# Performance work log

Measured on AMD Instinct MI355X. Metric: run time of the kernel, lower is better.

The kernel has to match this reference:

```python
import jax, jax.numpy as jnp
import numpy as np

B, S, D, H = 4, 2048, 1024, 16
DK = D // H

def setup_inputs() -> dict:
    key = jax.random.key(0)
    ks = jax.random.split(key, 5)
    std = np.sqrt(2.0 / (D + D)).astype(np.float32)
    return {
        "x": jax.random.normal(ks[0], (B, S, D), dtype=jnp.float32),
        "W_q": jax.random.normal(ks[1], (D, D), dtype=jnp.float32) * std,
        "W_k": jax.random.normal(ks[2], (D, D), dtype=jnp.float32) * std,
        "W_v": jax.random.normal(ks[3], (D, D), dtype=jnp.float32) * std,
        "W_o": jax.random.normal(ks[4], (D, D), dtype=jnp.float32) * std,
    }

def reference(x, W_q, W_k, W_v, W_o):
    b, s, d = x.shape
    # Linear layers: y = x @ W.T  (W stored as [out, in])
    q = (x @ W_q.T).reshape(b, s, H, DK).transpose(0, 2, 1, 3)  # [b,h,s,dk]
    k = (x @ W_k.T).reshape(b, s, H, DK).transpose(0, 2, 1, 3)
    v = (x @ W_v.T).reshape(b, s, H, DK).transpose(0, 2, 1, 3)
    scale = 1.0 / jnp.sqrt(jnp.asarray(DK, dtype=x.dtype))
    scores = jnp.einsum("bhqd,bhkd->bhqk", q, k) * scale  # [b,h,s,s]
    causal = jnp.tril(jnp.ones((s, s), dtype=bool))
    scores = jnp.where(causal, scores, jnp.asarray(-jnp.inf, dtype=scores.dtype))
    attn = jax.nn.softmax(scores, axis=-1)
    out = jnp.einsum("bhqk,bhkd->bhqd", attn, v)  # [b,h,s,dk]
    out = out.transpose(0, 2, 1, 3).reshape(b, s, d)
    return out @ W_o.T
```

## Files before the change

kernel.cpp:

```cpp
#include <hip/hip_runtime.h>
#include <stdint.h>

#define B_  4
#define S_  2048
#define D_  1024
#define H_  16
#define DK_ 64
#define M_  (B_ * S_)

typedef __attribute__((ext_vector_type(4))) float  f32x4;
typedef __attribute__((ext_vector_type(8))) __bf16 bf16x8;
typedef __attribute__((ext_vector_type(4))) unsigned short us4;

__device__ __forceinline__ unsigned short cvt_bf16(float f) {
  unsigned u = __float_as_uint(f);
  return (unsigned short)((u + 0x7fffu + ((u >> 16) & 1u)) >> 16);
}

__device__ __forceinline__ f32x4 mfma16(bf16x8 a, bf16x8 b, f32x4 c) {
  return __builtin_amdgcn_mfma_f32_16x16x32_bf16(a, b, c, 0, 0, 0);
}

__device__ __forceinline__ void async16(const void* g, void* l) {
  __builtin_amdgcn_global_load_lds(
      (const __attribute__((address_space(1))) void*)g,
      (__attribute__((address_space(3))) void*)l, 16, 0, 0);
}

#define XN4_ 2097152
#define WN4_ 262144
__global__ void cast_all(const float* __restrict__ x,
                         const float* __restrict__ wq,
                         const float* __restrict__ wk,
                         const float* __restrict__ wv,
                         const float* __restrict__ wo,
                         unsigned short* __restrict__ dst) {
  const int i = blockIdx.x * blockDim.x + threadIdx.x;
  const float* src;
  int k;
  if (i < XN4_) {
    src = x; k = i;
  } else {
    const int j = i - XN4_;
    const int wsel = j >> 18;
    k = j & (WN4_ - 1);
    src = (wsel == 0) ? wq : (wsel == 1) ? wk : (wsel == 2) ? wv : wo;
  }
  f32x4 v = ((const f32x4*)src)[k];
  us4 o;
  o[0] = cvt_bf16(v[0]); o[1] = cvt_bf16(v[1]);
  o[2] = cvt_bf16(v[2]); o[3] = cvt_bf16(v[3]);
  ((us4*)dst)[i] = o;
}

template <int OUTMODE>
__global__ __launch_bounds__(256) void gemm_bt(
    const unsigned short* __restrict__ A,
    const unsigned short* __restrict__ Bm,
    void* __restrict__ Cp,
    unsigned short* __restrict__ Qo, unsigned short* __restrict__ Ko,
    unsigned short* __restrict__ Vto,
    int Ndim, int Kdim) {
  constexpr int BM = 128, BN = 128, BK = 32;
  __shared__ __align__(16) unsigned short As[BM * BK];
  __shared__ __align__(16) unsigned short Bs[BN * BK];

  const int tid = threadIdx.x;
  const int w = tid >> 6, l = tid & 63;
  const int l16 = l & 15, lg = l >> 4;
  const int wr = w >> 1, wc = w & 1;
  const int rowA0 = blockIdx.y * BM;
  const int rowB0 = blockIdx.x * BN;
  const int l4 = l >> 2;
  const int lk = (l & 3) * 8;

  f32x4 acc[4][4] = {};

  for (int kt = 0; kt < Kdim; kt += BK) {
#pragma unroll
    for (int j = 0; j < 2; ++j) {
      const int chunk = j * 4 + w;
      const int r = chunk * 16 + l4;
      async16(A  + (size_t)(rowA0 + r) * Kdim + kt + lk, &As[chunk * 512]);
      async16(Bm + (size_t)(rowB0 + r) * Kdim + kt + lk, &Bs[chunk * 512]);
    }
    __syncthreads();
    bf16x8 af[4], bfr[4];
#pragma unroll
    for (int m = 0; m < 4; ++m)
      af[m] = *(const bf16x8*)&As[(wr * 64 + m * 16 + l16) * BK + lg * 8];
#pragma unroll
    for (int n = 0; n < 4; ++n)
      bfr[n] = *(const bf16x8*)&Bs[(wc * 64 + n * 16 + l16) * BK + lg * 8];
#pragma unroll
    for (int m = 0; m < 4; ++m)
#pragma unroll
      for (int n = 0; n < 4; ++n)
        acc[m][n] = mfma16(af[m], bfr[n], acc[m][n]);
    __syncthreads();
  }

  const int rb = rowA0 + wr * 64;
  const int cb = rowB0 + wc * 64;
  if constexpr (OUTMODE == 2) {
    float* C = (float*)Cp;
#pragma unroll
    for (int m = 0; m < 4; ++m)
#pragma unroll
      for (int n = 0; n < 4; ++n) {
        const int r0 = rb + m * 16 + lg * 4;
        const int c0 = cb + n * 16 + l16;
#pragma unroll
        for (int j = 0; j < 4; ++j)
          C[(size_t)(r0 + j) * Ndim + c0] = acc[m][n][j];
      }
  } else {
    const int region = cb >> 10;
    const int cbl = cb & 1023;
    if (region < 2) {
      unsigned short* C = region ? Ko : Qo;
#pragma unroll
      for (int m = 0; m < 4; ++m)
#pragma unroll
        for (int n = 0; n < 4; ++n) {
          const int r0 = rb + m * 16 + lg * 4;
          const int c0 = cbl + n * 16 + l16;
#pragma unroll
          for (int j = 0; j < 4; ++j)
            C[(size_t)(r0 + j) * 1024 + c0] = cvt_bf16(acc[m][n][j]);
        }
    } else {
#pragma unroll
      for (int m = 0; m < 4; ++m)
#pragma unroll
        for (int n = 0; n < 4; ++n) {
          const int r0 = rb + m * 16 + lg * 4;
          const int c0 = cbl + n * 16 + l16;
          us4 v;
#pragma unroll
          for (int j = 0; j < 4; ++j) v[j] = cvt_bf16(acc[m][n][j]);
          *(us4*)&Vto[((size_t)(r0 >> 11) * 1024 + c0) * 2048 + (r0 & 2047)] = v;
        }
    }
  }
}


#define KS_ 0.1803368801f

#define SMX(sc, mr, sr, oa, P, diag, rb, kv0)                                \
  do {                                                                       \
    if (diag) {                                                              \
      _Pragma("unroll") for (int nc_ = 0; nc_ < 4; ++nc_) {                  \
        const int col_ = (kv0) + nc_ * 16 + l16;                             \
        _Pragma("unroll") for (int j_ = 0; j_ < 4; ++j_)                     \
            if (col_ > (rb) + j_) sc[nc_][j_] = -INFINITY;                   \
      }                                                                      \
    }                                                                        \
    _Pragma("unroll") for (int j_ = 0; j_ < 4; ++j_) {                       \
      float t_ = fmaxf(fmaxf(sc[0][j_], sc[1][j_]),                          \
                       fmaxf(sc[2][j_], sc[3][j_]));                         \
      t_ = fmaxf(t_, __shfl_xor(t_, 1));                                     \
      t_ = fmaxf(t_, __shfl_xor(t_, 2));                                     \
      t_ = fmaxf(t_, __shfl_xor(t_, 4));                                     \
      t_ = fmaxf(t_, __shfl_xor(t_, 8));                                     \
      const bool st_ = __all(t_ <= mr[j_]);     \
      const float mnew_ = st_ ? mr[j_] : fmaxf(mr[j_], t_);                  \
      float rs_ = 0.f;                                                       \
      _Pragma("unroll") for (int nc_ = 0; nc_ < 4; ++nc_) {                  \
        const float p_ = exp2f((sc[nc_][j_] - mnew_) * KS_);                 \
        rs_ += p_;                                                           \
        P[lg * 4 + j_][nc_ * 16 + l16] = cvt_bf16(p_);                       \
      }                                                                      \
      rs_ += __shfl_xor(rs_, 1);                                             \
      rs_ += __shfl_xor(rs_, 2);                                             \
      rs_ += __shfl_xor(rs_, 4);                                             \
      rs_ += __shfl_xor(rs_, 8);                                             \
      if (st_) {                                                             \
        sr[j_] += rs_;                                                       \
      } else {                                                               \
        const float al_ = exp2f((mr[j_] - mnew_) * KS_);                     \
        sr[j_] = sr[j_] * al_ + rs_;                                         \
        mr[j_] = mnew_;                                                      \
        _Pragma("unroll") for (int d_ = 0; d_ < 4; ++d_) oa[d_][j_] *= al_;  \
      }                                                                      \
    }                                                                        \
  } while (0)

__global__ __launch_bounds__(256, 4) void flash_attn(
    const unsigned short* __restrict__ Q,
    const unsigned short* __restrict__ K,
    const unsigned short* __restrict__ Vt,
    unsigned short* __restrict__ O) {
  const int bid  = blockIdx.x;
  const int virt = (bid & 7) * 128 + (bid >> 3);
  const int bh   = virt >> 4;
  const int x    = virt & 15;
  const int b = bh >> 4, h = bh & 15;
  const int tid = threadIdx.x;
  const int w = tid >> 6, l = tid & 63;
  const int l16 = l & 15, lg = l >> 4;

  __shared__ __align__(16) unsigned short Ks[64 * 64];
  __shared__ __align__(16) unsigned short Vs[64 * 64];
  __shared__ __align__(16) unsigned short PA[4][16][72];
  __shared__ __align__(16) unsigned short PB[4][16][72];

  const int tA = x, tB = 31 - x;

  const size_t qkbase = (size_t)(b * S_) * D_ + h * DK_;
  const size_t vbase  = ((size_t)(b * D_) + h * DK_) * S_;

  const int rA = tA * 64 + w * 16 + l16;
  const int rB = tB * 64 + w * 16 + l16;
  bf16x8 qfA[2], qfB[2];
  qfA[0] = *(const bf16x8*)&Q[qkbase + (size_t)rA * D_ + lg * 8];
  qfA[1] = *(const bf16x8*)&Q[qkbase + (size_t)rA * D_ + 32 + lg * 8];
  qfB[0] = *(const bf16x8*)&Q[qkbase + (size_t)rB * D_ + lg * 8];
  qfB[1] = *(const bf16x8*)&Q[qkbase + (size_t)rB * D_ + 32 + lg * 8];

  float mA[4], sA[4], mB[4], sB[4];
  f32x4 oA[4] = {}, oB[4] = {};
#pragma unroll
  for (int j = 0; j < 4; ++j) {
    mA[j] = mB[j] = -INFINITY;
    sA[j] = sB[j] = 0.f;
  }

  const int rbA = tA * 64 + w * 16 + lg * 4;
  const int rbB = tB * 64 + w * 16 + lg * 4;

  for (int kv = 0; kv <= tB; ++kv) {
    const int kv0 = kv * 64;
    if (kv) __syncthreads();
#pragma unroll
    for (int c = 0; c < 2; ++c) {
      const int ci = c * 256 + w * 64;
      const int i  = ci + l;
      const int r  = i >> 3;
      const int cc = (i & 7) ^ (r & 7);
      async16(K  + qkbase + (size_t)(kv0 + r) * D_ + cc * 8, &Ks[ci * 8]);
      async16(Vt + vbase  + (size_t)r * S_ + kv0 + cc * 8,   &Vs[ci * 8]);
    }
    __syncthreads();

    if (kv <= tA) {
      f32x4 sc[4] = {};
      __builtin_amdgcn_s_setprio(1);
#pragma unroll
      for (int nc = 0; nc < 4; ++nc) {
        const int r = nc * 16 + l16;
#pragma unroll
        for (int ks = 0; ks < 2; ++ks) {
          const int byte = (r * 128 + ks * 64 + lg * 16) ^ ((r & 7) << 4);
          bf16x8 kf = *(const bf16x8*)((const char*)Ks + byte);
          sc[nc] = mfma16(qfA[ks], kf, sc[nc]);
        }
      }
      __builtin_amdgcn_s_setprio(0);
      SMX(sc, mA, sA, oA, PA[w], kv == tA, rbA, kv0);
      __asm__ volatile("s_waitcnt lgkmcnt(0)" ::: "memory");
      bf16x8 pa0 = *(const bf16x8*)&PA[w][l16][lg * 8];
      bf16x8 pa1 = *(const bf16x8*)&PA[w][l16][32 + lg * 8];
      __builtin_amdgcn_s_setprio(1);
#pragma unroll
      for (int d = 0; d < 4; ++d) {
        const int r = d * 16 + l16;
#pragma unroll
        for (int ks = 0; ks < 2; ++ks) {
          const int byte = (r * 128 + ks * 64 + lg * 16) ^ ((r & 7) << 4);
          bf16x8 vf = *(const bf16x8*)((const char*)Vs + byte);
          oA[d] = mfma16(ks ? pa1 : pa0, vf, oA[d]);
        }
      }
      __builtin_amdgcn_s_setprio(0);
    }

    {
      f32x4 sc[4] = {};
      __builtin_amdgcn_s_setprio(1);
#pragma unroll
      for (int nc = 0; nc < 4; ++nc) {
        const int r = nc * 16 + l16;
#pragma unroll
        for (int ks = 0; ks < 2; ++ks) {
          const int byte = (r * 128 + ks * 64 + lg * 16) ^ ((r & 7) << 4);
          bf16x8 kf = *(const bf16x8*)((const char*)Ks + byte);
          sc[nc] = mfma16(qfB[ks], kf, sc[nc]);
        }
      }
      __builtin_amdgcn_s_setprio(0);
      SMX(sc, mB, sB, oB, PB[w], kv == tB, rbB, kv0);
      __asm__ volatile("s_waitcnt lgkmcnt(0)" ::: "memory");
      bf16x8 pb0 = *(const bf16x8*)&PB[w][l16][lg * 8];
      bf16x8 pb1 = *(const bf16x8*)&PB[w][l16][32 + lg * 8];
      __builtin_amdgcn_s_setprio(1);
#pragma unroll
      for (int d = 0; d < 4; ++d) {
        const int r = d * 16 + l16;
#pragma unroll
        for (int ks = 0; ks < 2; ++ks) {
          const int byte = (r * 128 + ks * 64 + lg * 16) ^ ((r & 7) << 4);
          bf16x8 vf = *(const bf16x8*)((const char*)Vs + byte);
          oB[d] = mfma16(ks ? pb1 : pb0, vf, oB[d]);
        }
      }
      __builtin_amdgcn_s_setprio(0);
    }
  }

#pragma unroll
  for (int j = 0; j < 4; ++j) {
    const float iA = __builtin_amdgcn_rcpf(sA[j]);
    const float iB = __builtin_amdgcn_rcpf(sB[j]);
#pragma unroll
    for (int d = 0; d < 4; ++d) {
      O[((size_t)(b * S_) + rbA + j) * D_ + h * DK_ + d * 16 + l16] =
          cvt_bf16(oA[d][j] * iA);
      O[((size_t)(b * S_) + rbB + j) * D_ + h * DK_ + d * 16 + l16] =
          cvt_bf16(oB[d][j] * iB);
    }
  }
}

extern "C" void kernel_launch(void* const* d_in, const int* in_sizes, int n_in,
                              void* d_out, int out_size, void* d_ws,
                              size_t ws_size, hipStream_t stream) {
  const float* x  = (const float*)d_in[0];
  const float* Wq = (const float*)d_in[1];
  const float* Wk = (const float*)d_in[2];
  const float* Wv = (const float*)d_in[3];
  const float* Wo = (const float*)d_in[4];

  const size_t XN = (size_t)M_ * D_;
  const size_t WN = (size_t)D_ * D_;
  unsigned short* xb  = (unsigned short*)d_ws;
  unsigned short* Wqb = xb + XN;
  unsigned short* Wob = Wqb + 3 * WN;
  unsigned short* Qb  = Wob + WN;
  unsigned short* Kb  = Qb + XN;
  unsigned short* Vtb = Kb + XN;
  unsigned short* Ob  = Vtb + XN;

  cast_all<<<(XN4_ + 4 * WN4_) / 256, 256, 0, stream>>>(x, Wq, Wk, Wv, Wo, xb);

  gemm_bt<3><<<dim3(24, 64), 256, 0, stream>>>(xb, Wqb, nullptr, Qb, Kb, Vtb,
                                               3072, D_);

  flash_attn<<<dim3(1024), 256, 0, stream>>>(Qb, Kb, Vtb, Ob);

  gemm_bt<2><<<dim3(8, 64), 256, 0, stream>>>(Ob, Wob, d_out, nullptr, nullptr,
                                              nullptr, D_, D_);
}
```

Before: 318.2 us.

## Double-buffer K/V tiles and interleave both query tiles per KV step

After: 410.1 us. +28.9%, slower.

```diff
diff --git a/kernel.cpp b/kernel.cpp
--- a/kernel.cpp
+++ b/kernel.cpp
@@ -187,7 +187,22 @@
     }                                                                        \
   } while (0)
 
-__global__ __launch_bounds__(256, 4) void flash_attn(
+#define STAGE(kvt, pb)                                                       \
+  do {                                                                       \
+    const int kv0_ = (kvt) * 64;                                             \
+    _Pragma("unroll") for (int c_ = 0; c_ < 2; ++c_) {                       \
+      const int ci_ = c_ * 256 + w * 64;                                     \
+      const int i_  = ci_ + l;                                               \
+      const int r_  = i_ >> 3;                                               \
+      const int cc_ = (i_ & 7) ^ (r_ & 7);                                   \
+      async16(K  + qkbase + (size_t)(kv0_ + r_) * D_ + cc_ * 8,              \
+              &Ks[pb][ci_ * 8]);                                             \
+      async16(Vt + vbase  + (size_t)r_ * S_ + kv0_ + cc_ * 8,                \
+              &Vs[pb][ci_ * 8]);                                             \
+    }                                                                        \
+  } while (0)
+
+__global__ __launch_bounds__(256, 3) void flash_attn(
     const unsigned short* __restrict__ Q,
     const unsigned short* __restrict__ K,
     const unsigned short* __restrict__ Vt,
@@ -201,8 +216,8 @@
   const int w = tid >> 6, l = tid & 63;
   const int l16 = l & 15, lg = l >> 4;
 
-  __shared__ __align__(16) unsigned short Ks[64 * 64];
-  __shared__ __align__(16) unsigned short Vs[64 * 64];
+  __shared__ __align__(16) unsigned short Ks[2][64 * 64];
+  __shared__ __align__(16) unsigned short Vs[2][64 * 64];
   __shared__ __align__(16) unsigned short PA[4][16][72];
   __shared__ __align__(16) unsigned short PB[4][16][72];
 
@@ -230,83 +245,55 @@
   const int rbA = tA * 64 + w * 16 + lg * 4;
   const int rbB = tB * 64 + w * 16 + lg * 4;
 
+  STAGE(0, 0);
+  __syncthreads();
+
   for (int kv = 0; kv <= tB; ++kv) {
+    const int p = kv & 1;
     const int kv0 = kv * 64;
-    if (kv) __syncthreads();
-#pragma unroll
-    for (int c = 0; c < 2; ++c) {
-      const int ci = c * 256 + w * 64;
-      const int i  = ci + l;
-      const int r  = i >> 3;
-      const int cc = (i & 7) ^ (r & 7);
-      async16(K  + qkbase + (size_t)(kv0 + r) * D_ + cc * 8, &Ks[ci * 8]);
-      async16(Vt + vbase  + (size_t)r * S_ + kv0 + cc * 8,   &Vs[ci * 8]);
+    if (kv < tB) STAGE(kv + 1, p ^ 1);
+
+    const bool doA = (kv <= tA);
+    const char* Kp = (const char*)&Ks[p][0];
+    const char* Vp = (const char*)&Vs[p][0];
+
+    f32x4 scA[4] = {}, scB[4] = {};
+#pragma unroll
+    for (int nc = 0; nc < 4; ++nc) {
+      const int r = nc * 16 + l16;
+#pragma unroll
+      for (int ks = 0; ks < 2; ++ks) {
+        const int byte = (r * 128 + ks * 64 + lg * 16) ^ ((r & 7) << 4);
+        bf16x8 kf = *(const bf16x8*)(Kp + byte);
+        if (doA) scA[nc] = mfma16(qfA[ks], kf, scA[nc]);
+        scB[nc] = mfma16(qfB[ks], kf, scB[nc]);
+      }
+    }
+
+    if (doA) SMX(scA, mA, sA, oA, PA[w], kv == tA, rbA, kv0);
+    SMX(scB, mB, sB, oB, PB[w], kv == tB, rbB, kv0);
+
+    __asm__ volatile("s_waitcnt lgkmcnt(0)" ::: "memory");
+    bf16x8 paA0, paA1, paB0, paB1;
+    if (doA) {
+      paA0 = *(const bf16x8*)&PA[w][l16][lg * 8];
+      paA1 = *(const bf16x8*)&PA[w][l16][32 + lg * 8];
+    }
+    paB0 = *(const bf16x8*)&PB[w][l16][lg * 8];
+    paB1 = *(const bf16x8*)&PB[w][l16][32 + lg * 8];
+
+#pragma unroll
+    for (int d = 0; d < 4; ++d) {
+      const int r = d * 16 + l16;
+#pragma unroll
+      for (int ks = 0; ks < 2; ++ks) {
+        const int byte = (r * 128 + ks * 64 + lg * 16) ^ ((r & 7) << 4);
+        bf16x8 vf = *(const bf16x8*)(Vp + byte);
+        if (doA) oA[d] = mfma16(ks ? paA1 : paA0, vf, oA[d]);
+        oB[d] = mfma16(ks ? paB1 : paB0, vf, oB[d]);
+      }
     }
     __syncthreads();
-
-    if (kv <= tA) {
-      f32x4 sc[4] = {};
-      __builtin_amdgcn_s_setprio(1);
-#pragma unroll
-      for (int nc = 0; nc < 4; ++nc) {
-        const int r = nc * 16 + l16;
-#pragma unroll
-        for (int ks = 0; ks < 2; ++ks) {
-          const int byte = (r * 128 + ks * 64 + lg * 16) ^ ((r & 7) << 4);
-          bf16x8 kf = *(const bf16x8*)((const char*)Ks + byte);
-          sc[nc] = mfma16(qfA[ks], kf, sc[nc]);
-        }
-      }
-      __builtin_amdgcn_s_setprio(0);
-      SMX(sc, mA, sA, oA, PA[w], kv == tA, rbA, kv0);
-      __asm__ volatile("s_waitcnt lgkmcnt(0)" ::: "memory");
-      bf16x8 pa0 = *(const bf16x8*)&PA[w][l16][lg * 8];
-      bf16x8 pa1 = *(const bf16x8*)&PA[w][l16][32 + lg * 8];
-      __builtin_amdgcn_s_setprio(1);
-#pragma unroll
-      for (int d = 0; d < 4; ++d) {
-        const int r = d * 16 + l16;
-#pragma unroll
-        for (int ks = 0; ks < 2; ++ks) {
-          const int byte = (r * 128 + ks * 64 + lg * 16) ^ ((r & 7) << 4);
-          bf16x8 vf = *(const bf16x8*)((const char*)Vs + byte);
-          oA[d] = mfma16(ks ? pa1 : pa0, vf, oA[d]);
-        }
-      }
-      __builtin_amdgcn_s_setprio(0);
-    }
-
-    {
-      f32x4 sc[4] = {};
-      __builtin_amdgcn_s_setprio(1);
-#pragma unroll
-      for (int nc = 0; nc < 4; ++nc) {
-        const int r = nc * 16 + l16;
-#pragma unroll
-        for (int ks = 0; ks < 2; ++ks) {
-          const int byte = (r * 128 + ks * 64 + lg * 16) ^ ((r & 7) << 4);
-          bf16x8 kf = *(const bf16x8*)((const char*)Ks + byte);
-          sc[nc] = mfma16(qfB[ks], kf, sc[nc]);
-        }
-      }
-      __builtin_amdgcn_s_setprio(0);
-      SMX(sc, mB, sB, oB, PB[w], kv == tB, rbB, kv0);
-      __asm__ volatile("s_waitcnt lgkmcnt(0)" ::: "memory");
-      bf16x8 pb0 = *(const bf16x8*)&PB[w][l16][lg * 8];
-      bf16x8 pb1 = *(const bf16x8*)&PB[w][l16][32 + lg * 8];
-      __builtin_amdgcn_s_setprio(1);
-#pragma unroll
-      for (int d = 0; d < 4; ++d) {
-        const int r = d * 16 + l16;
-#pragma unroll
-        for (int ks = 0; ks < 2; ++ks) {
-          const int byte = (r * 128 + ks * 64 + lg * 16) ^ ((r & 7) << 4);
-          bf16x8 vf = *(const bf16x8*)((const char*)Vs + byte);
-          oB[d] = mfma16(ks ? pb1 : pb0, vf, oB[d]);
-        }
-      }
-      __builtin_amdgcn_s_setprio(0);
-    }
   }
 
 #pragma unroll
```
